# Optimization experiments

Hardware: AMD Instinct MI355X
Metric: run time of the kernel (lower is better)

## Reference

```python
import jax, jax.numpy as jnp
import numpy as np

N = 12
C = 512
THRED = 0.1
NEG_SLOPE = 0.2

ADJ_BASE = jnp.asarray(np.array([
    [0,0,0,1,0,1,1,1,1,1,1,1],
    [0,0,0,1,0,1,1,1,1,1,1,1],
    [0,0,0,1,0,1,1,1,1,1,1,1],
    [1,1,1,0,1,1,1,1,1,1,1,1],
    [0,0,0,1,0,1,1,1,1,1,1,1],
    [1,1,1,1,1,0,1,1,1,0,0,0],
    [1,1,1,1,1,1,0,0,0,1,1,1],
    [1,1,1,1,1,1,0,0,0,1,1,1],
    [1,1,1,1,1,1,0,0,0,1,1,1],
    [1,1,1,1,1,0,1,1,1,0,0,0],
    [1,1,1,1,1,0,1,1,1,0,0,0],
    [1,1,1,1,1,0,1,1,1,0,0,0]], dtype=np.float32))


def setup_inputs() -> dict:
    key = jax.random.key(0)
    k1, k2, k3, k4, k5 = jax.random.split(key, 5)
    B = 16384
    x = jax.random.normal(k1, (B, N, C), dtype=jnp.float32)
    adj_mask = jax.random.uniform(k2, (B, N, N), dtype=jnp.float32)
    s = 1.0 / jnp.sqrt(jnp.float32(C))
    W = jax.random.normal(k3, (C, C), dtype=jnp.float32) * s
    a_l = jax.random.normal(k4, (C,), dtype=jnp.float32) * s
    a_r = jax.random.normal(k5, (C,), dtype=jnp.float32) * s
    return {"x": x, "adj_mask": adj_mask, "W": W, "a_l": a_l, "a_r": a_r}


def reference(x, adj_mask, W, a_l, a_r):
    # adj = base * mask + I  (self loops)
    adj = ADJ_BASE[None, :, :] * adj_mask + jnp.eye(N, dtype=x.dtype)[None]  # [B,N,N]
    # single-head GAT: project, compute additive attention logits
    h = jnp.einsum('bnc,cd->bnd', x, W)          # [B,N,C]
    el = jnp.einsum('bnd,d->bn', h, a_l)         # [B,N]
    er = jnp.einsum('bnd,d->bn', h, a_r)         # [B,N]
    e = jax.nn.leaky_relu(el[:, :, None] + er[:, None, :], NEG_SLOPE)  # [B,N,N]
    mask = adj > THRED
    e = jnp.where(mask, e, jnp.finfo(x.dtype).min)
    alpha = jax.nn.softmax(e, axis=-1)           # masked softmax over neighbors
    out = jnp.einsum('bnm,bmd->bnd', alpha, h)   # aggregate
    return out + x                               # residual (in==out)
```

## Files before the change

### kernel.cpp

```cpp
#include <hip/hip_runtime.h>
#include <stdint.h>

typedef float f32x4 __attribute__((ext_vector_type(4)));
typedef short s16x8 __attribute__((ext_vector_type(8)));

__device__ __forceinline__ unsigned int fpack2(float a, float b){
  unsigned int ua = __float_as_uint(a); ua += 0x7FFFu + ((ua >> 16) & 1u);
  unsigned int ub = __float_as_uint(b); ub += 0x7FFFu + ((ub >> 16) & 1u);
  return (ua >> 16) | (ub & 0xFFFF0000u);
}
__device__ __forceinline__ unsigned short f2bf(float f){
  unsigned int u = __float_as_uint(f);
  u += 0x7FFFu + ((u >> 16) & 1u);
  return (unsigned short)(u >> 16);
}

__global__ __launch_bounds__(256) void k_pack_w(const float* __restrict__ W,
                                                unsigned short* __restrict__ wp){
  int idx = blockIdx.x * 256 + threadIdx.x;
  int k = idx >> 9, n = idx & 511;
  int kt = k >> 5, kr = k & 31;
  int q  = kr >> 3, j = kr & 7;
  int ntg = n >> 4, c = n & 15;
  wp[((kt*32 + ntg)*64 + q*16 + c)*8 + j] = f2bf(W[idx]);
}

__global__ __launch_bounds__(256, 2) void k_gat(
    const float* __restrict__ x, const float* __restrict__ adjm,
    const unsigned short* __restrict__ wp,
    const float* __restrict__ al, const float* __restrict__ ar,
    float* __restrict__ out)
{
  const int tid  = threadIdx.x;
  const int lane = tid & 63;
  const int wv   = tid >> 6;
  const int c16  = lane & 15;
  const int quad = lane >> 4;
  const int wg   = blockIdx.x;
  const int R0   = wg * 48;

  __shared__ __align__(16) unsigned short a_lds[2][1536];
  __shared__ __align__(16) unsigned short hpack[8192];
  __shared__ __align__(16) unsigned short alpha_lds[1024];
  __shared__ float elw[4][48];
  __shared__ float erw[4][48];

  f32x4 acc[3][8];
  const f32x4 zero4 = {0.f, 0.f, 0.f, 0.f};
  const s16x8 zero8 = {0,0,0,0,0,0,0,0};
#pragma unroll
  for (int i = 0; i < 3; i++)
#pragma unroll
    for (int j = 0; j < 8; j++) acc[i][j] = zero4;

  const int srow = tid >> 2;
  const int sq   = tid & 3;
  const bool stager = (tid < 192);
  const float* xsrc = x + (R0 + srow) * 512 + sq * 8;
  const int adst = (srow >> 4) * 64 + sq * 16 + (srow & 15);

  const s16x8* wps = (const s16x8*)wp;
  s16x8 breg[2][8];

#pragma unroll
  for (int nt = 0; nt < 8; nt++) breg[0][nt] = wps[(wv*8 + nt)*64 + lane];
  if (stager){
    uint4 v;
    v.x = fpack2(xsrc[0], xsrc[1]); v.y = fpack2(xsrc[2], xsrc[3]);
    v.z = fpack2(xsrc[4], xsrc[5]); v.w = fpack2(xsrc[6], xsrc[7]);
    ((uint4*)a_lds[0])[adst] = v;
  }
  __syncthreads();

#pragma unroll
  for (int kt = 0; kt < 16; ++kt){
    const int buf = kt & 1;
    if (kt < 15){
#pragma unroll
      for (int nt = 0; nt < 8; nt++)
        breg[buf^1][nt] = wps[((kt+1)*32 + wv*8 + nt)*64 + lane];
    }
    float xr[8];
    if (kt < 15 && stager){
      const float* p = xsrc + (kt+1)*32;
#pragma unroll
      for (int i = 0; i < 8; i++) xr[i] = p[i];
    }
    s16x8 af[3];
#pragma unroll
    for (int mt = 0; mt < 3; mt++) af[mt] = ((const s16x8*)a_lds[buf])[mt*64 + lane];
#pragma unroll
    for (int mt = 0; mt < 3; mt++)
#pragma unroll
      for (int nt = 0; nt < 8; nt++)
        acc[mt][nt] = __builtin_amdgcn_mfma_f32_16x16x32_bf16(af[mt], breg[buf][nt], acc[mt][nt], 0, 0, 0);
    if (kt < 15 && stager){
      uint4 v;
      v.x = fpack2(xr[0], xr[1]); v.y = fpack2(xr[2], xr[3]);
      v.z = fpack2(xr[4], xr[5]); v.w = fpack2(xr[6], xr[7]);
      ((uint4*)a_lds[buf^1])[adst] = v;
    }
    __syncthreads();
  }

  float alv[8], arv[8];
#pragma unroll
  for (int nt = 0; nt < 8; nt++){
    int col = wv*128 + nt*16 + c16;
    alv[nt] = al[col]; arv[nt] = ar[col];
  }
#pragma unroll
  for (int mt = 0; mt < 3; mt++){
#pragma unroll
    for (int r = 0; r < 4; r++){
      float sl = 0.f, sr = 0.f;
#pragma unroll
      for (int nt = 0; nt < 8; nt++){
        float v = acc[mt][nt][r];
        sl += v * alv[nt]; sr += v * arv[nt];
      }
#pragma unroll
      for (int off = 1; off < 16; off <<= 1){
        sl += __shfl_xor(sl, off, 64);
        sr += __shfl_xor(sr, off, 64);
      }
      if (c16 == 0){
        int g = mt*16 + quad*4 + r;
        elw[wv][g] = sl; erw[wv][g] = sr;
      }
    }
  }
  {
    uint4 z4; z4.x = z4.y = z4.z = z4.w = 0u;
    if (tid < 128) ((uint4*)alpha_lds)[tid] = z4;
#pragma unroll
    for (int i = 0; i < 2; i++){
      int p = tid + 256*i;
      int ntg = p >> 4, s = 16 + (p & 15);
      uint2 z2; z2.x = 0u; z2.y = 0u;
      *(uint2*)&hpack[(ntg*32 + s)*8 + 4] = z2;
    }
  }
  __syncthreads();

  if (lane < 12){
    const int n = lane;
    float el_ = elw[0][wv*12+n] + elw[1][wv*12+n] + elw[2][wv*12+n] + elw[3][wv*12+n];
    float er_ = erw[0][wv*12+n] + erw[1][wv*12+n] + erw[2][wv*12+n] + erw[3][wv*12+n];
    const unsigned long long W0 = 0x0FF70FE80FE80FE8ull;
    const unsigned long long W1 = 0x0E3F0E3F01DF0FE8ull;
    const unsigned long long W2 = 0x01DF01DF01DF0E3Full;
    unsigned long long wrow = (n < 4) ? W0 : ((n < 8) ? W1 : W2);
    unsigned rowm = (unsigned)((wrow >> ((n & 3) * 16)) & 0xFFFu);
    const float* am = adjm + (long)(wg*4 + wv) * 144 + n * 12;
    float e[12]; float mx = -3.0e38f;
#pragma unroll
    for (int m = 0; m < 12; m++){
      float erm = __shfl(er_, m, 64);
      float z = el_ + erm;
      z = (z > 0.f) ? z : 0.2f * z;
      bool ok = (m == n) || ((((rowm >> m) & 1u) != 0u) && (am[m] > 0.1f));
      e[m] = ok ? z : -3.0e38f;
      mx = fmaxf(mx, e[m]);
    }
    float s = 0.f; float pr[12];
#pragma unroll
    for (int m = 0; m < 12; m++){
      float p = (e[m] > -1.0e38f) ? __expf(e[m] - mx) : 0.f;
      pr[m] = p; s += p;
    }
    float inv = 1.0f / s;
#pragma unroll
    for (int m = 0; m < 12; m++)
      alpha_lds[(wv*16 + n)*16 + m] = f2bf(pr[m] * inv);
  }
  __syncthreads();

#pragma unroll
  for (int t = 0; t < 4; t++){
#pragma unroll
    for (int mt = 0; mt < 3; mt++){
      int r0 = mt*16 + quad*4;
      int bi = r0 / 12;
      if (bi == t){
        int kb0 = r0 - bi*12;
        int qp  = kb0 >> 3;
        int j0  = kb0 & 7;
#pragma unroll
        for (int nt = 0; nt < 8; nt++){
          int ntg = wv*8 + nt;
          uint2 v;
          v.x = fpack2(acc[mt][nt][0], acc[mt][nt][1]);
          v.y = fpack2(acc[mt][nt][2], acc[mt][nt][3]);
          *(uint2*)&hpack[(ntg*32 + qp*16 + c16)*8 + j0] = v;
        }
      }
    }
    __syncthreads();
    {
      s16x8 aA = zero8;
      if (quad < 2) aA = *(const s16x8*)&alpha_lds[(t*16 + c16)*16 + quad*8];
#pragma unroll
      for (int nt = 0; nt < 8; nt++){
        int ntg = wv*8 + nt;
        s16x8 bB = zero8;
        if (quad < 2) bB = *(const s16x8*)&hpack[(ntg*32 + lane)*8];
        f32x4 r4 = __builtin_amdgcn_mfma_f32_16x16x32_bf16(aA, bB, zero4, 0, 0, 0);
        if (quad < 3){
          int base = (R0 + t*12 + quad*4)*512 + ntg*16 + c16;
#pragma unroll
          for (int r = 0; r < 4; r++){
            int a2 = base + r*512;
            out[a2] = r4[r] + x[a2];
          }
        }
      }
    }
    if (t < 3) __syncthreads();
  }
}

extern "C" void kernel_launch(void* const* d_in, const int* in_sizes, int n_in,
                              void* d_out, int out_size, void* d_ws, size_t ws_size,
                              hipStream_t stream) {
  const float* x    = (const float*)d_in[0];
  const float* adjm = (const float*)d_in[1];
  const float* W    = (const float*)d_in[2];
  const float* al   = (const float*)d_in[3];
  const float* ar   = (const float*)d_in[4];
  float* out = (float*)d_out;
  unsigned short* wp = (unsigned short*)d_ws;

  k_pack_w<<<1024, 256, 0, stream>>>(W, wp);
  k_gat<<<4096, 256, 0, stream>>>(x, adjm, wp, al, ar, out);
}
```

Before: 869.6 us.

## Stage whole x tile into LDS upfront and drop per-k-step barriers

```diff
diff --git a/kernel.cpp b/kernel.cpp
--- a/kernel.cpp
+++ b/kernel.cpp
@@ -25,7 +25,7 @@
   wp[((kt*32 + ntg)*64 + q*16 + c)*8 + j] = f2bf(W[idx]);
 }
 
-__global__ __launch_bounds__(256, 2) void k_gat(
+__global__ __launch_bounds__(256, 3) void k_gat(
     const float* __restrict__ x, const float* __restrict__ adjm,
     const unsigned short* __restrict__ wp,
     const float* __restrict__ al, const float* __restrict__ ar,
@@ -39,11 +39,40 @@
   const int wg   = blockIdx.x;
   const int R0   = wg * 48;
 
-  __shared__ __align__(16) unsigned short a_lds[2][1536];
-  __shared__ __align__(16) unsigned short hpack[8192];
-  __shared__ __align__(16) unsigned short alpha_lds[1024];
-  __shared__ float elw[4][48];
-  __shared__ float erw[4][48];
+  __shared__ __align__(16) unsigned char smem[49152];
+  uint4* stage = (uint4*)smem;
+  unsigned short* hpack = (unsigned short*)smem;
+  unsigned short* alpha = (unsigned short*)(smem + 16384);
+  float* elw = (float*)(smem + 18432);
+  float* erw = (float*)(smem + 19200);
+
+  f32x4 xr[24];
+  {
+    const float* xb = x + (long)R0 * 512;
+#pragma unroll
+    for (int i = 0; i < 12; i++){
+      int c = tid + 256*i;
+      int row = c >> 6, kc = c & 63;
+      const float* p = xb + row*512 + kc*8;
+      xr[2*i]   = *(const f32x4*)p;
+      xr[2*i+1] = *(const f32x4*)(p + 4);
+    }
+#pragma unroll
+    for (int i = 0; i < 12; i++){
+      int c = tid + 256*i;
+      int row = c >> 6, kc = c & 63;
+      int kt = kc >> 2, q = kc & 3;
+      int mt = row >> 4, cc = row & 15;
+      int idx = ((kt*3 + mt) << 6) + (q << 4) + (cc ^ q ^ ((kt & 3) << 2));
+      uint4 v;
+      v.x = fpack2(xr[2*i][0], xr[2*i][1]);
+      v.y = fpack2(xr[2*i][2], xr[2*i][3]);
+      v.z = fpack2(xr[2*i+1][0], xr[2*i+1][1]);
+      v.w = fpack2(xr[2*i+1][2], xr[2*i+1][3]);
+      stage[idx] = v;
+    }
+  }
+  __syncthreads();
 
   f32x4 acc[3][8];
   const f32x4 zero4 = {0.f, 0.f, 0.f, 0.f};
@@ -53,55 +82,24 @@
 #pragma unroll
     for (int j = 0; j < 8; j++) acc[i][j] = zero4;
 
-  const int srow = tid >> 2;
-  const int sq   = tid & 3;
-  const bool stager = (tid < 192);
-  const float* xsrc = x + (R0 + srow) * 512 + sq * 8;
-  const int adst = (srow >> 4) * 64 + sq * 16 + (srow & 15);
-
   const s16x8* wps = (const s16x8*)wp;
-  s16x8 breg[2][8];
-
-#pragma unroll
-  for (int nt = 0; nt < 8; nt++) breg[0][nt] = wps[(wv*8 + nt)*64 + lane];
-  if (stager){
-    uint4 v;
-    v.x = fpack2(xsrc[0], xsrc[1]); v.y = fpack2(xsrc[2], xsrc[3]);
-    v.z = fpack2(xsrc[4], xsrc[5]); v.w = fpack2(xsrc[6], xsrc[7]);
-    ((uint4*)a_lds[0])[adst] = v;
-  }
-  __syncthreads();
-
+  const s16x8* sp  = (const s16x8*)smem;
 #pragma unroll
   for (int kt = 0; kt < 16; ++kt){
-    const int buf = kt & 1;
-    if (kt < 15){
+    s16x8 breg[8];
+#pragma unroll
+    for (int nt = 0; nt < 8; nt++)
+      breg[nt] = wps[(kt*32 + wv*8 + nt)*64 + lane];
+    const int cxs = c16 ^ quad ^ ((kt & 3) << 2);
+#pragma unroll
+    for (int mt = 0; mt < 3; mt++){
+      s16x8 af = sp[((kt*3 + mt) << 6) + (quad << 4) + cxs];
 #pragma unroll
       for (int nt = 0; nt < 8; nt++)
-        breg[buf^1][nt] = wps[((kt+1)*32 + wv*8 + nt)*64 + lane];
-    }
-    float xr[8];
-    if (kt < 15 && stager){
-      const float* p = xsrc + (kt+1)*32;
-#pragma unroll
-      for (int i = 0; i < 8; i++) xr[i] = p[i];
-    }
-    s16x8 af[3];
-#pragma unroll
-    for (int mt = 0; mt < 3; mt++) af[mt] = ((const s16x8*)a_lds[buf])[mt*64 + lane];
-#pragma unroll
-    for (int mt = 0; mt < 3; mt++)
-#pragma unroll
-      for (int nt = 0; nt < 8; nt++)
-        acc[mt][nt] = __builtin_amdgcn_mfma_f32_16x16x32_bf16(af[mt], breg[buf][nt], acc[mt][nt], 0, 0, 0);
-    if (kt < 15 && stager){
-      uint4 v;
-      v.x = fpack2(xr[0], xr[1]); v.y = fpack2(xr[2], xr[3]);
-      v.z = fpack2(xr[4], xr[5]); v.w = fpack2(xr[6], xr[7]);
-      ((uint4*)a_lds[buf^1])[adst] = v;
-    }
-    __syncthreads();
-  }
+        acc[mt][nt] = __builtin_amdgcn_mfma_f32_16x16x32_bf16(af, breg[nt], acc[mt][nt], 0, 0, 0);
+    }
+  }
+  __syncthreads();
 
   float alv[8], arv[8];
 #pragma unroll
@@ -126,13 +124,13 @@
       }
       if (c16 == 0){
         int g = mt*16 + quad*4 + r;
-        elw[wv][g] = sl; erw[wv][g] = sr;
+        elw[wv*48 + g] = sl; erw[wv*48 + g] = sr;
       }
     }
   }
   {
     uint4 z4; z4.x = z4.y = z4.z = z4.w = 0u;
-    if (tid < 128) ((uint4*)alpha_lds)[tid] = z4;
+    if (tid < 128) ((uint4*)alpha)[tid] = z4;
 #pragma unroll
     for (int i = 0; i < 2; i++){
       int p = tid + 256*i;
@@ -145,8 +143,8 @@
 
   if (lane < 12){
     const int n = lane;
-    float el_ = elw[0][wv*12+n] + elw[1][wv*12+n] + elw[2][wv*12+n] + elw[3][wv*12+n];
-    float er_ = erw[0][wv*12+n] + erw[1][wv*12+n] + erw[2][wv*12+n] + erw[3][wv*12+n];
+    float el_ = elw[0*48 + wv*12+n] + elw[1*48 + wv*12+n] + elw[2*48 + wv*12+n] + elw[3*48 + wv*12+n];
+    float er_ = erw[0*48 + wv*12+n] + erw[1*48 + wv*12+n] + erw[2*48 + wv*12+n] + erw[3*48 + wv*12+n];
     const unsigned long long W0 = 0x0FF70FE80FE80FE8ull;
     const unsigned long long W1 = 0x0E3F0E3F01DF0FE8ull;
     const unsigned long long W2 = 0x01DF01DF01DF0E3Full;
@@ -172,7 +170,7 @@
     float inv = 1.0f / s;
 #pragma unroll
     for (int m = 0; m < 12; m++)
-      alpha_lds[(wv*16 + n)*16 + m] = f2bf(pr[m] * inv);
+      alpha[(wv*16 + n)*16 + m] = f2bf(pr[m] * inv);
   }
   __syncthreads();
 
@@ -199,7 +197,7 @@
     __syncthreads();
     {
       s16x8 aA = zero8;
-      if (quad < 2) aA = *(const s16x8*)&alpha_lds[(t*16 + c16)*16 + quad*8];
+      if (quad < 2) aA = *(const s16x8*)&alpha[(t*16 + c16)*16 + quad*8];
 #pragma unroll
       for (int nt = 0; nt < 8; nt++){
         int ntg = wv*8 + nt;
```

Result: faster. 807.0 us (-7.2%).
